# Kernel optimization log

Measured on AMD Instinct MI355X. Metric: run time of the kernel, lower is better.

## Reference

```python
import jax, jax.numpy as jnp
import numpy as np

EPS = 1e-08


def _center(K):
    # H K H with H = I - 11^T/n, expressed as O(n^2) double mean-subtraction
    rm = K.mean(axis=-1, keepdims=True)
    cm = K.mean(axis=-2, keepdims=True)
    tm = K.mean(axis=(-1, -2), keepdims=True)
    return K - rm - cm + tm


def setup_inputs() -> dict:
    key = jax.random.key(0)
    k1, k2 = jax.random.split(key)
    L, B, n, d = 5, 8, 1024, 64
    teacher = jax.random.normal(k1, (L, B, n, d), dtype=jnp.float32)
    student = jax.random.normal(k2, (L, B, n, d), dtype=jnp.float32)
    return {"teacher": teacher, "student": student}


def reference(teacher, student):
    # teacher, student: [L, B, n, d]  (internal=True, dim>=3 branch)
    cX = _center(jnp.einsum('lbnd,lbmd->lbnm', teacher, teacher))  # [L,B,n,n]
    cY = _center(jnp.einsum('lbnd,lbmd->lbnm', student, student))  # [L,B,n,n]
    hsic_xy = jnp.sum(cX * cY, axis=(-1, -2))  # [L,B]
    var_x = jnp.sqrt(jnp.sum(cX * cX, axis=(-1, -2)))  # [L,B]
    var_y = jnp.sqrt(jnp.sum(cY * cY, axis=(-1, -2)))  # [L,B]
    ratio = jnp.abs(hsic_xy / (var_x * var_y))  # [L,B]
    loss_per_layer = -jnp.log(ratio.mean(axis=-1) + EPS)  # [L]
    return loss_per_layer.mean()  # sum over layers / length
```

## Files before the change

### kernel.cpp

```cpp
#include <hip/hip_runtime.h>
#include <math.h>

#define LL 5
#define BB 8
#define NN 1024
#define DD 64
#define LB 40
#define SPLIT 16
#define KC (NN / SPLIT)
#define ZC (2 * DD)
#define NQ 3

#define GP_SHORTS (LB * SPLIT * NQ * 4096)
#define GP_FLOATS (GP_SHORTS / 2)
#define SP_OFF GP_FLOATS
#define ACC_OFF (GP_FLOATS + LB * SPLIT * ZC)
#define CNT_OFF (ACC_OFF + LB * 12)

typedef short short8 __attribute__((ext_vector_type(8)));
typedef float floatx4 __attribute__((ext_vector_type(4)));

__device__ __forceinline__ unsigned short f2bf(float f) {
    union { float f; unsigned u; } v; v.f = f;
    const unsigned u = v.u;
    return (unsigned short)((u + 0x7FFFu + ((u >> 16) & 1u)) >> 16);
}
__device__ __forceinline__ float bf2f(unsigned short h) {
    union { unsigned u; float f; } v; v.u = ((unsigned)h) << 16; return v.f;
}
__device__ __forceinline__ float bflo(unsigned u) {
    union { unsigned u; float f; } v; v.u = u << 16; return v.f;
}
__device__ __forceinline__ float bfhi(unsigned u) {
    union { unsigned u; float f; } v; v.u = u & 0xFFFF0000u; return v.f;
}

__device__ __forceinline__ short8 read_frag(const short* Zt, int tbase, int lane, int k0) {
    const int c = tbase + (lane & 15);
    const int o = (k0 >> 3) + (lane >> 4);
    const int oct = (o ^ ((c + (c >> 4)) & 15)) & 7;
    return *(const short8*)(Zt + c * 64 + (oct << 3));
}

__global__ __launch_bounds__(256) void gram_kernel(const float* __restrict__ X,
                                                   const float* __restrict__ Y,
                                                   unsigned* __restrict__ Gp,
                                                   float* __restrict__ Sp,
                                                   unsigned* __restrict__ cnt) {
    __shared__ short Zt[ZC * KC];
    __shared__ float cscr[8][ZC];

    const int lb = blockIdx.y, nc = blockIdx.x, tid = threadIdx.x;
    const int r0 = nc * KC;
    const float4* X4 = (const float4*)(X + (size_t)lb * NN * DD);
    const float4* Y4 = (const float4*)(Y + (size_t)lb * NN * DD);

    if (blockIdx.x == 0 && blockIdx.y == 0 && tid == 0) *cnt = 0u;

    const int col4 = tid & 31;
    const int rb = tid >> 5;
    float4 v[8];
#pragma unroll
    for (int m = 0; m < 8; ++m) {
        const int row = 8 * rb + m;
        v[m] = (col4 < 16) ? X4[(size_t)(r0 + row) * 16 + col4]
                           : Y4[(size_t)(r0 + row) * 16 + (col4 - 16)];
    }

#pragma unroll
    for (int e = 0; e < 4; ++e) {
        const int c = 4 * col4 + e;
        short8 w8;
        float cs = 0.f;
#pragma unroll
        for (int m = 0; m < 8; ++m) {
            const float fv = (e == 0) ? v[m].x : (e == 1) ? v[m].y : (e == 2) ? v[m].z : v[m].w;
            const unsigned short b = f2bf(fv);
            cs += bf2f(b);
            w8[m] = (short)b;
        }
        const int oct = (rb ^ ((c + (c >> 4)) & 15)) & 7;
        *(short8*)(Zt + c * 64 + (oct << 3)) = w8;
        cscr[rb][c] = cs;
    }
    __syncthreads();
    if (tid < ZC) {
        float s = 0.f;
#pragma unroll
        for (int g = 0; g < 8; ++g) s += cscr[g][tid];
        Sp[(lb * SPLIT + nc) * ZC + tid] = s;
    }

    const int lane = tid & 63, w = tid >> 6;
    const int jbeg = (w < 2) ? 0 : 4;

    floatx4 acc[2][8];
#pragma unroll
    for (int i = 0; i < 2; ++i)
#pragma unroll
        for (int j = 0; j < 8; ++j) acc[i][j] = (floatx4){0.f, 0.f, 0.f, 0.f};

#pragma unroll
    for (int k0 = 0; k0 < KC; k0 += 32) {
        short8 af[2], bfr[8];
#pragma unroll
        for (int i = 0; i < 2; ++i) af[i] = read_frag(Zt, (2 * w + i) * 16, lane, k0);
#pragma unroll
        for (int j = 0; j < 8; ++j)
            if (j >= jbeg) bfr[j] = read_frag(Zt, j * 16, lane, k0);
#pragma unroll
        for (int i = 0; i < 2; ++i)
#pragma unroll
            for (int j = 0; j < 8; ++j)
                if (j >= jbeg)
                    acc[i][j] = __builtin_amdgcn_mfma_f32_16x16x32_bf16(af[i], bfr[j], acc[i][j], 0, 0, 0);
    }

    unsigned* Gb = Gp + (size_t)(lb * SPLIT + nc) * (NQ * 2048);
    const int g = lane >> 4, cl = lane & 15;
#pragma unroll
    for (int i = 0; i < 2; ++i)
#pragma unroll
        for (int j = 0; j < 8; ++j) {
            if (j < jbeg) continue;
            const int slab = (w < 2) ? ((j < 4) ? 0 : 1) : 2;
            const int qrow0 = (w < 2 ? (2 * w + i) : (2 * (w - 2) + i)) * 16 + g * 4;
            const int qcol = (j & 3) * 16 + cl;
            const unsigned lo = (unsigned)f2bf(acc[i][j][0]) | ((unsigned)f2bf(acc[i][j][1]) << 16);
            const unsigned hi = (unsigned)f2bf(acc[i][j][2]) | ((unsigned)f2bf(acc[i][j][3]) << 16);
            Gb[slab * 2048 + (qrow0 >> 1) * 64 + qcol] = lo;
            Gb[slab * 2048 + ((qrow0 >> 1) + 1) * 64 + qcol] = hi;
        }
}

__global__ __launch_bounds__(256) void reduce_kernel(const unsigned* __restrict__ Gp,
                                                     const float* __restrict__ Sp,
                                                     float* __restrict__ Acc2,
                                                     unsigned* __restrict__ cnt,
                                                     float* __restrict__ out) {
    const int b = blockIdx.x;
    const int lb = b / (NQ * 4);
    const int rem = b % (NQ * 4);
    const int q = rem >> 2, seg = rem & 3;
    const int tid = threadIdx.x;

    __shared__ float stot[ZC];
    __shared__ float red[4];
    __shared__ unsigned lastflag;

    if (tid < ZC) {
        float s = 0.f;
#pragma unroll
        for (int sp = 0; sp < SPLIT; ++sp) s += Sp[(lb * SPLIT + sp) * ZC + tid];
        stot[tid] = s;
    }
    __syncthreads();

    const int u0 = seg * 512 + tid * 2;
    const int rp = u0 >> 6;
    const int c0 = u0 & 63;

    float g00 = 0.f, g10 = 0.f, g01 = 0.f, g11 = 0.f;
#pragma unroll
    for (int sp = 0; sp < SPLIT; ++sp) {
        const uint2 p = *(const uint2*)&Gp[((size_t)(lb * SPLIT + sp) * NQ + q) * 2048 + u0];
        g00 += bflo(p.x); g10 += bfhi(p.x);
        g01 += bflo(p.y); g11 += bfhi(p.y);
    }
    const int rowbase = (q == 2) ? 64 : 0;
    const int colbase = (q == 0) ? 0 : 64;
    const float inv_n = 1.0f / (float)NN;
    const float sr0 = stot[rowbase + 2 * rp] * inv_n;
    const float sr1 = stot[rowbase + 2 * rp + 1] * inv_n;
    const float sc0 = stot[colbase + c0];
    const float sc1 = stot[colbase + c0 + 1];
    float sq = 0.f;
    { const float cv = g00 - sr0 * sc0; sq += cv * cv; }
    { const float cv = g10 - sr1 * sc0; sq += cv * cv; }
    { const float cv = g01 - sr0 * sc1; sq += cv * cv; }
    { const float cv = g11 - sr1 * sc1; sq += cv * cv; }

#pragma unroll
    for (int off = 32; off; off >>= 1) sq += __shfl_down(sq, off);
    const int wave = tid >> 6;
    if ((tid & 63) == 0) red[wave] = sq;
    __syncthreads();

    if (tid == 0) {
        Acc2[lb * 12 + q * 4 + seg] = red[0] + red[1] + red[2] + red[3];
        __threadfence();
        const unsigned old = atomicAdd(cnt, 1u);
        lastflag = (old == (unsigned)(LB * NQ * 4 - 1)) ? 1u : 0u;
    }
    __syncthreads();

    if (lastflag && tid < 64) {
        __threadfence();
        float v = 0.f;
        if (tid < LB) {
            float vxx = 0.f, hxy = 0.f, vyy = 0.f;
#pragma unroll
            for (int s = 0; s < 4; ++s) {
                vxx += __hip_atomic_load(Acc2 + tid * 12 + s, __ATOMIC_RELAXED, __HIP_MEMORY_SCOPE_AGENT);
                hxy += __hip_atomic_load(Acc2 + tid * 12 + 4 + s, __ATOMIC_RELAXED, __HIP_MEMORY_SCOPE_AGENT);
                vyy += __hip_atomic_load(Acc2 + tid * 12 + 8 + s, __ATOMIC_RELAXED, __HIP_MEMORY_SCOPE_AGENT);
            }
            v = fabsf(hxy / (sqrtf(vxx) * sqrtf(vyy)));
        }
        v += __shfl_xor(v, 1);
        v += __shfl_xor(v, 2);
        v += __shfl_xor(v, 4);
        float loss = 0.f;
#pragma unroll
        for (int l = 0; l < LL; ++l) {
            const float sl = __shfl(v, l * BB);
            loss += -logf(sl * (1.0f / (float)BB) + 1e-8f);
        }
        if (tid == 0) out[0] = loss * (1.0f / (float)LL);
    }
}

extern "C" void kernel_launch(void* const* d_in, const int* in_sizes, int n_in,
                              void* d_out, int out_size, void* d_ws, size_t ws_size,
                              hipStream_t stream) {
    const float* teacher = (const float*)d_in[0];
    const float* student = (const float*)d_in[1];
    float* ws = (float*)d_ws;
    unsigned* Gp = (unsigned*)ws;
    float* Sp = ws + SP_OFF;
    float* Acc2 = ws + ACC_OFF;
    unsigned* cnt = (unsigned*)(ws + CNT_OFF);

    dim3 grid1(SPLIT, LB);
    gram_kernel<<<grid1, 256, 0, stream>>>(teacher, student, Gp, Sp, cnt);
    reduce_kernel<<<LB * NQ * 4, 256, 0, stream>>>(Gp, Sp, Acc2, cnt, (float*)d_out);
}
```

Baseline: 87.76 us.

## Fuse gram and reduce kernels via per-lb last-block completion counters

Merges the two kernels into one. The last of the SPLIT blocks for each (l,b) pair, detected with an atomic counter, performs that pair's centered-norm reduction over all three quadrants. A global counter then lets the final block compute the loss. This removes a kernel launch and its inter-kernel gap, but the reduction for each lb is now serialized onto a single block (12 segments instead of 12 blocks), and a memset is added to reset the counters.

After: 148.1 us. +68.8%, slower.

```diff
diff --git a/kernel.cpp b/kernel.cpp
--- a/kernel.cpp
+++ b/kernel.cpp
@@ -11,11 +11,10 @@
 #define ZC (2 * DD)
 #define NQ 3
 
-#define GP_SHORTS (LB * SPLIT * NQ * 4096)
-#define GP_FLOATS (GP_SHORTS / 2)
-#define SP_OFF GP_FLOATS
-#define ACC_OFF (GP_FLOATS + LB * SPLIT * ZC)
-#define CNT_OFF (ACC_OFF + LB * 12)
+#define GP_UINTS (LB * SPLIT * NQ * 2048)
+#define SP_OFF GP_UINTS
+#define RATIO_OFF (SP_OFF + LB * SPLIT * ZC)
+#define CNT_OFF (RATIO_OFF + LB)
 
 typedef short short8 __attribute__((ext_vector_type(8)));
 typedef float floatx4 __attribute__((ext_vector_type(4)));
@@ -42,20 +41,24 @@
     return *(const short8*)(Zt + c * 64 + (oct << 3));
 }
 
-__global__ __launch_bounds__(256) void gram_kernel(const float* __restrict__ X,
-                                                   const float* __restrict__ Y,
-                                                   unsigned* __restrict__ Gp,
-                                                   float* __restrict__ Sp,
-                                                   unsigned* __restrict__ cnt) {
+__global__ __launch_bounds__(256) void fused_kernel(const float* __restrict__ X,
+                                                    const float* __restrict__ Y,
+                                                    unsigned* __restrict__ Gp,
+                                                    float* __restrict__ Sp,
+                                                    float* __restrict__ Ratio,
+                                                    unsigned* __restrict__ cnt_lb,
+                                                    unsigned* __restrict__ gcnt,
+                                                    float* __restrict__ out) {
     __shared__ short Zt[ZC * KC];
     __shared__ float cscr[8][ZC];
+    __shared__ float stot[ZC];
+    __shared__ float red3[4][3];
+    __shared__ unsigned lflag, gflag;
 
     const int lb = blockIdx.y, nc = blockIdx.x, tid = threadIdx.x;
     const int r0 = nc * KC;
     const float4* X4 = (const float4*)(X + (size_t)lb * NN * DD);
     const float4* Y4 = (const float4*)(Y + (size_t)lb * NN * DD);
-
-    if (blockIdx.x == 0 && blockIdx.y == 0 && tid == 0) *cnt = 0u;
 
     const int col4 = tid & 31;
     const int rb = tid >> 5;
@@ -131,22 +134,17 @@
             Gb[slab * 2048 + (qrow0 >> 1) * 64 + qcol] = lo;
             Gb[slab * 2048 + ((qrow0 >> 1) + 1) * 64 + qcol] = hi;
         }
-}
-
-__global__ __launch_bounds__(256) void reduce_kernel(const unsigned* __restrict__ Gp,
-                                                     const float* __restrict__ Sp,
-                                                     float* __restrict__ Acc2,
-                                                     unsigned* __restrict__ cnt,
-                                                     float* __restrict__ out) {
-    const int b = blockIdx.x;
-    const int lb = b / (NQ * 4);
-    const int rem = b % (NQ * 4);
-    const int q = rem >> 2, seg = rem & 3;
-    const int tid = threadIdx.x;
-
-    __shared__ float stot[ZC];
-    __shared__ float red[4];
-    __shared__ unsigned lastflag;
+
+    __syncthreads();
+    if (tid == 0) {
+        __threadfence();
+        const unsigned old = atomicAdd(&cnt_lb[lb], 1u);
+        lflag = (old == SPLIT - 1) ? 1u : 0u;
+    }
+    __syncthreads();
+    if (!lflag) return;
+
+    __threadfence();
 
     if (tid < ZC) {
         float s = 0.f;
@@ -156,57 +154,61 @@
     }
     __syncthreads();
 
-    const int u0 = seg * 512 + tid * 2;
-    const int rp = u0 >> 6;
-    const int c0 = u0 & 63;
-
-    float g00 = 0.f, g10 = 0.f, g01 = 0.f, g11 = 0.f;
-#pragma unroll
-    for (int sp = 0; sp < SPLIT; ++sp) {
-        const uint2 p = *(const uint2*)&Gp[((size_t)(lb * SPLIT + sp) * NQ + q) * 2048 + u0];
-        g00 += bflo(p.x); g10 += bfhi(p.x);
-        g01 += bflo(p.y); g11 += bfhi(p.y);
-    }
-    const int rowbase = (q == 2) ? 64 : 0;
-    const int colbase = (q == 0) ? 0 : 64;
+    const unsigned* Gq = Gp + (size_t)lb * SPLIT * (NQ * 2048);
     const float inv_n = 1.0f / (float)NN;
-    const float sr0 = stot[rowbase + 2 * rp] * inv_n;
-    const float sr1 = stot[rowbase + 2 * rp + 1] * inv_n;
-    const float sc0 = stot[colbase + c0];
-    const float sc1 = stot[colbase + c0 + 1];
-    float sq = 0.f;
-    { const float cv = g00 - sr0 * sc0; sq += cv * cv; }
-    { const float cv = g10 - sr1 * sc0; sq += cv * cv; }
-    { const float cv = g01 - sr0 * sc1; sq += cv * cv; }
-    { const float cv = g11 - sr1 * sc1; sq += cv * cv; }
-
-#pragma unroll
-    for (int off = 32; off; off >>= 1) sq += __shfl_down(sq, off);
-    const int wave = tid >> 6;
-    if ((tid & 63) == 0) red[wave] = sq;
+    float sq3[3] = {0.f, 0.f, 0.f};
+#pragma unroll
+    for (int q = 0; q < NQ; ++q) {
+        const int rowbase = (q == 2) ? 64 : 0;
+        const int colbase = (q == 0) ? 0 : 64;
+#pragma unroll
+        for (int seg = 0; seg < 4; ++seg) {
+            const int u0 = seg * 512 + tid * 2;
+            const int rp = u0 >> 6;
+            const int c0 = u0 & 63;
+            float g00 = 0.f, g10 = 0.f, g01 = 0.f, g11 = 0.f;
+#pragma unroll
+            for (int sp = 0; sp < SPLIT; ++sp) {
+                const uint2 p = *(const uint2*)&Gq[((size_t)sp * NQ + q) * 2048 + u0];
+                g00 += bflo(p.x); g10 += bfhi(p.x);
+                g01 += bflo(p.y); g11 += bfhi(p.y);
+            }
+            const float sr0 = stot[rowbase + 2 * rp] * inv_n;
+            const float sr1 = stot[rowbase + 2 * rp + 1] * inv_n;
+            const float sc0 = stot[colbase + c0];
+            const float sc1 = stot[colbase + c0 + 1];
+            { const float cv = g00 - sr0 * sc0; sq3[q] += cv * cv; }
+            { const float cv = g10 - sr1 * sc0; sq3[q] += cv * cv; }
+            { const float cv = g01 - sr0 * sc1; sq3[q] += cv * cv; }
+            { const float cv = g11 - sr1 * sc1; sq3[q] += cv * cv; }
+        }
+    }
+#pragma unroll
+    for (int q = 0; q < NQ; ++q)
+#pragma unroll
+        for (int off = 32; off; off >>= 1) sq3[q] += __shfl_down(sq3[q], off);
+    if ((tid & 63) == 0) {
+#pragma unroll
+        for (int q = 0; q < NQ; ++q) red3[tid >> 6][q] = sq3[q];
+    }
     __syncthreads();
 
     if (tid == 0) {
-        Acc2[lb * 12 + q * 4 + seg] = red[0] + red[1] + red[2] + red[3];
+        const float vxx = red3[0][0] + red3[1][0] + red3[2][0] + red3[3][0];
+        const float hxy = red3[0][1] + red3[1][1] + red3[2][1] + red3[3][1];
+        const float vyy = red3[0][2] + red3[1][2] + red3[2][2] + red3[3][2];
+        Ratio[lb] = fabsf(hxy / (sqrtf(vxx) * sqrtf(vyy)));
         __threadfence();
-        const unsigned old = atomicAdd(cnt, 1u);
-        lastflag = (old == (unsigned)(LB * NQ * 4 - 1)) ? 1u : 0u;
-    }
-    __syncthreads();
-
-    if (lastflag && tid < 64) {
+        const unsigned old = atomicAdd(gcnt, 1u);
+        gflag = (old == LB - 1) ? 1u : 0u;
+    }
+    __syncthreads();
+
+    if (gflag && tid < 64) {
         __threadfence();
         float v = 0.f;
-        if (tid < LB) {
-            float vxx = 0.f, hxy = 0.f, vyy = 0.f;
-#pragma unroll
-            for (int s = 0; s < 4; ++s) {
-                vxx += __hip_atomic_load(Acc2 + tid * 12 + s, __ATOMIC_RELAXED, __HIP_MEMORY_SCOPE_AGENT);
-                hxy += __hip_atomic_load(Acc2 + tid * 12 + 4 + s, __ATOMIC_RELAXED, __HIP_MEMORY_SCOPE_AGENT);
-                vyy += __hip_atomic_load(Acc2 + tid * 12 + 8 + s, __ATOMIC_RELAXED, __HIP_MEMORY_SCOPE_AGENT);
-            }
-            v = fabsf(hxy / (sqrtf(vxx) * sqrtf(vyy)));
-        }
+        if (tid < LB)
+            v = __hip_atomic_load(Ratio + tid, __ATOMIC_RELAXED, __HIP_MEMORY_SCOPE_AGENT);
         v += __shfl_xor(v, 1);
         v += __shfl_xor(v, 2);
         v += __shfl_xor(v, 4);
@@ -228,10 +230,12 @@
     float* ws = (float*)d_ws;
     unsigned* Gp = (unsigned*)ws;
     float* Sp = ws + SP_OFF;
-    float* Acc2 = ws + ACC_OFF;
-    unsigned* cnt = (unsigned*)(ws + CNT_OFF);
+    float* Ratio = ws + RATIO_OFF;
+    unsigned* cnt = (unsigned*)ws + CNT_OFF;
+
+    hipMemsetAsync((void*)cnt, 0, (LB + 1) * sizeof(unsigned), stream);
 
     dim3 grid1(SPLIT, LB);
-    gram_kernel<<<grid1, 256, 0, stream>>>(teacher, student, Gp, Sp, cnt);
-    reduce_kernel<<<LB * NQ * 4, 256, 0, stream>>>(Gp, Sp, Acc2, cnt, (float*)d_out);
-}
+    fused_kernel<<<grid1, 256, 0, stream>>>(teacher, student, Gp, Sp, Ratio,
+                                            cnt, cnt + LB, (float*)d_out);
+}
```
